# Kernel optimization log

Measured on AMD Instinct MI355X. Metric: run time of the kernel, lower is better.

The kernel has to match this reference:

```python
import jax, jax.numpy as jnp
import numpy as np

N, B, SDIM, ADIM, HID, HEADS = 8, 32768, 128, 16, 128, 4
AD = HID // HEADS  # attend_dim = 32
IDIM = SDIM + ADIM


def setup_inputs() -> dict:
    key = jax.random.key(0)
    ks = jax.random.split(key, 16)
    nrm = jax.random.normal
    return {
        "states": nrm(ks[0], (N, B, SDIM), jnp.float32),
        "actions": nrm(ks[1], (N, B, ADIM), jnp.float32),
        # per-agent critic encoder (Linear(idim, hid) + ReLU)
        "We": nrm(ks[2], (N, IDIM, HID), jnp.float32) * 0.05,
        "be": nrm(ks[3], (N, HID), jnp.float32) * 0.05,
        # per-agent state encoder (Linear(sdim, hid) + ReLU)
        "Ws": nrm(ks[4], (N, SDIM, HID), jnp.float32) * 0.05,
        "bs": nrm(ks[5], (N, HID), jnp.float32) * 0.05,
        # per-head extractors (shared across agents)
        "Wk": nrm(ks[6], (HEADS, HID, AD), jnp.float32) * 0.05,  # bias=False
        "Wq": nrm(ks[7], (HEADS, HID, AD), jnp.float32) * 0.05,  # bias=False
        "Wv": nrm(ks[8], (HEADS, HID, AD), jnp.float32) * 0.05,
        "bv": nrm(ks[9], (HEADS, AD), jnp.float32) * 0.05,
        # per-agent critic head: Linear(2*hid, hid) + ReLU + Linear(hid, adim)
        "Wc1": nrm(ks[10], (N, 2 * HID, HID), jnp.float32) * 0.05,
        "bc1": nrm(ks[11], (N, HID), jnp.float32) * 0.05,
        "Wc2": nrm(ks[12], (N, HID, ADIM), jnp.float32) * 0.05,
        "bc2": nrm(ks[13], (N, ADIM), jnp.float32) * 0.05,
    }


def reference(states, actions, We, be, Ws, bs, Wk, Wq, Wv, bv, Wc1, bc1, Wc2, bc2):
    # encoders
    inp = jnp.concatenate([states, actions], axis=-1)                      # [N,B,idim]
    sa_enc = jax.nn.relu(jnp.einsum('nbi,nih->nbh', inp, We) + be[:, None, :])
    s_enc = jax.nn.relu(jnp.einsum('nbs,nsh->nbh', states, Ws) + bs[:, None, :])
    # per-head keys/values/selectors; k = head index
    K = jnp.einsum('nbh,khd->knbd', sa_enc, Wk)                            # [H,N,B,ad]
    V = jax.nn.relu(jnp.einsum('nbh,khd->knbd', sa_enc, Wv) + bv[:, None, None, :])
    Q = jnp.einsum('nbh,khd->knbd', s_enc, Wq)
    # attention logits: selector of agent i dotted with key of agent j
    logits = jnp.einsum('kibd,kjbd->kbij', Q, K) / np.sqrt(AD).astype(np.float32)
    # exclude-self masking (equivalent to stacking keys with j != i)
    self_mask = jnp.eye(N, dtype=bool)                                     # [N,N]
    masked = jnp.where(self_mask[None, None, :, :], jnp.float32(-1e9), logits)
    attn = jax.nn.softmax(masked, axis=-1)                                 # [H,B,N,N]
    other = jnp.einsum('kbij,kjbd->ikbd', attn, V)                         # [N,H,B,ad]
    other = other.transpose(0, 2, 1, 3).reshape(N, B, HEADS * AD)          # head-order concat
    # per-agent critic MLP
    critic_in = jnp.concatenate([s_enc, other], axis=-1)                   # [N,B,2*hid]
    h1 = jax.nn.relu(jnp.einsum('nbc,nch->nbh', critic_in, Wc1) + bc1[:, None, :])
    all_q = jnp.einsum('nbh,nha->nba', h1, Wc2) + bc2[:, None, :]          # [N,B,adim]
    int_acs = jnp.argmax(actions, axis=-1)                                 # [N,B]
    q = jnp.take_along_axis(all_q, int_acs[..., None], axis=-1)            # [N,B,1]
    return q
```

## Files before the change

kernel.cpp:

```cpp
#include <hip/hip_runtime.h>

#define NAG 8
#define BB 32768
#define SDIM 128
#define ADIM 16
#define HID 128
#define IDIM 144

typedef unsigned short u16;
typedef unsigned int u32;
typedef __attribute__((ext_vector_type(8))) short short8;
typedef __attribute__((ext_vector_type(4))) float floatx4;

__device__ __forceinline__ u16 f2bf(float f) {
  u32 u = __float_as_uint(f);
  u32 r = (u + 0x7FFFu + ((u >> 16) & 1u)) >> 16;
  return (u16)r;
}
__device__ __forceinline__ float bflo(u32 u) { return __uint_as_float(u << 16); }
__device__ __forceinline__ float bfhi(u32 u) { return __uint_as_float(u & 0xFFFF0000u); }


__global__ void prep_kernel(const float* __restrict__ We, const float* __restrict__ Ws,
                            const float* __restrict__ Wk, const float* __restrict__ Wq,
                            const float* __restrict__ Wv, const float* __restrict__ Wc1,
                            u16* __restrict__ ws) {
  int idx = blockIdx.x * 256 + threadIdx.x;
  const float* src;
  u16* dst;
  int e, Kreal, mode = 0;
  if (idx < 163840) {
    int a = idx / 20480; e = idx % 20480;
    src = We + a * (IDIM * HID); dst = ws + a * 20480; Kreal = IDIM;
  } else if (idx < 294912) {
    int r = idx - 163840; int a = r >> 14; e = r & 16383;
    src = Ws + a * 16384; dst = ws + 163840 + a * 16384; Kreal = 128;
  } else if (idx < 311296) {
    e = idx - 294912; src = Wk; dst = ws + 294912; Kreal = 128; mode = 1;
  } else if (idx < 327680) {
    e = idx - 311296; src = Wv; dst = ws + 311296; Kreal = 128; mode = 1;
  } else if (idx < 344064) {
    e = idx - 327680; src = Wq; dst = ws + 327680; Kreal = 128; mode = 1;
  } else if (idx < 606208) {
    int r = idx - 344064; int a = r >> 15; e = r & 32767;
    src = Wc1 + a * 32768; dst = ws + 344064 + a * 32768; Kreal = 256;
  } else {
    return;
  }
  int j = e & 7, lane = (e >> 3) & 63, ct = (e >> 9) & 7, kc = e >> 12;
  int k = kc * 32 + ((lane >> 4) << 3) + j;
  int c = ct * 16 + (lane & 15);
  float val = 0.f;
  if (k < Kreal)
    val = mode ? src[((c >> 5) * 128 + k) * 32 + (c & 31)]
               : src[k * 128 + c];
  dst[e] = f2bf(val);
}

template <int NKC>
__device__ __forceinline__ void gemm8(const u16* A, const int astride, const u16* W,
                                      const int wave, const int lane, floatx4* acc) {
  const int arow = wave * 16 + (lane & 15);
  const int koff = (lane >> 4) << 3;
#pragma unroll
  for (int kc = 0; kc < NKC; ++kc) {
    short8 a = *(const short8*)&A[arow * astride + kc * 32 + koff];
#pragma unroll
    for (int ct = 0; ct < 8; ++ct) {
      short8 b = *(const short8*)&W[kc * 4096 + ct * 512 + lane * 8];
      acc[ct] = __builtin_amdgcn_mfma_f32_16x16x32_bf16(a, b, acc[ct], 0, 0, 0);
    }
  }
}

__global__ __launch_bounds__(512) void k1_kernel(
    const float* __restrict__ states, const float* __restrict__ actions,
    const float* __restrict__ be, const float* __restrict__ bs, const float* __restrict__ bv,
    const u16* __restrict__ wsbase,
    u16* __restrict__ Kbuf, u16* __restrict__ Vbuf, u16* __restrict__ Qbuf,
    u16* __restrict__ CI) {
  __shared__ __align__(16) u16 Alds[128 * 168];
  __shared__ __align__(16) u16 Wb[20480];
  __shared__ __align__(16) u16 E1[128 * 136];
  __shared__ __align__(16) u16 E2[128 * 136];

  const int tid = threadIdx.x, lane = tid & 63, wave = tid >> 6;
  const int n = blockIdx.y;
  const size_t b0 = (size_t)blockIdx.x * 128;
  const int colb = lane & 15;
  const int rowl = wave * 16 + ((lane >> 4) << 2);

  const u16* WeP = wsbase;
  const u16* WsP = wsbase + 163840;
  const u16* WkP = wsbase + 294912;
  const u16* WvP = wsbase + 311296;
  const u16* WqP = wsbase + 327680;

  {
    const float4* sp = (const float4*)(states + ((size_t)n * BB + b0) * SDIM);
#pragma unroll
    for (int it = 0; it < 8; ++it) {
      int c = tid + it * 512;
      float4 v = sp[c];
      int row = c >> 5, col = (c & 31) << 2;
      *(uint2*)&Alds[row * 168 + col] =
          make_uint2((u32)f2bf(v.x) | ((u32)f2bf(v.y) << 16),
                     (u32)f2bf(v.z) | ((u32)f2bf(v.w) << 16));
    }
    const float4* apt = (const float4*)(actions + ((size_t)n * BB + b0) * ADIM);
    {
      float4 v = apt[tid];
      int row = tid >> 2, col = 128 + ((tid & 3) << 2);
      *(uint2*)&Alds[row * 168 + col] =
          make_uint2((u32)f2bf(v.x) | ((u32)f2bf(v.y) << 16),
                     (u32)f2bf(v.z) | ((u32)f2bf(v.w) << 16));
    }
    {
      int row = tid >> 2, col = 144 + ((tid & 3) << 2);
      *(uint2*)&Alds[row * 168 + col] = make_uint2(0u, 0u);
    }
    const uint4* s4 = (const uint4*)(WeP + (size_t)n * 20480);
    uint4* d4 = (uint4*)Wb;
#pragma unroll
    for (int it = 0; it < 5; ++it) d4[tid + it * 512] = s4[tid + it * 512];
  }
  __syncthreads();

  floatx4 acc[8];

#pragma unroll
  for (int ct = 0; ct < 8; ++ct) acc[ct] = (floatx4){0.f, 0.f, 0.f, 0.f};
  gemm8<5>(Alds, 168, Wb, wave, lane, acc);
#pragma unroll
  for (int ct = 0; ct < 8; ++ct) {
    int col = ct * 16 + colb;
    float bb = be[n * HID + col];
#pragma unroll
    for (int r = 0; r < 4; ++r)
      E1[(rowl + r) * 136 + col] = f2bf(fmaxf(acc[ct][r] + bb, 0.f));
  }
  __syncthreads();
  {
    const uint4* s4 = (const uint4*)(WsP + (size_t)n * 16384);
    uint4* d4 = (uint4*)Wb;
#pragma unroll
    for (int it = 0; it < 4; ++it) d4[tid + it * 512] = s4[tid + it * 512];
  }
  __syncthreads();

#pragma unroll
  for (int ct = 0; ct < 8; ++ct) acc[ct] = (floatx4){0.f, 0.f, 0.f, 0.f};
  gemm8<4>(Alds, 168, Wb, wave, lane, acc);
#pragma unroll
  for (int ct = 0; ct < 8; ++ct) {
    int col = ct * 16 + colb;
    float bb = bs[n * HID + col];
#pragma unroll
    for (int r = 0; r < 4; ++r) {
      u16 u = f2bf(fmaxf(acc[ct][r] + bb, 0.f));
      E2[(rowl + r) * 136 + col] = u;
      CI[((size_t)n * BB + b0 + rowl + r) * 256 + col] = u;
    }
  }
  __syncthreads();
  {
    const uint4* s4 = (const uint4*)WkP;
    uint4* d4 = (uint4*)Wb;
#pragma unroll
    for (int it = 0; it < 4; ++it) d4[tid + it * 512] = s4[tid + it * 512];
  }
  __syncthreads();

#pragma unroll
  for (int ct = 0; ct < 8; ++ct) acc[ct] = (floatx4){0.f, 0.f, 0.f, 0.f};
  gemm8<4>(E1, 136, Wb, wave, lane, acc);
#pragma unroll
  for (int ct = 0; ct < 8; ++ct) {
    int col = ct * 16 + colb;
#pragma unroll
    for (int r = 0; r < 4; ++r)
      Kbuf[((size_t)n * BB + b0 + rowl + r) * HID + col] = f2bf(acc[ct][r]);
  }
  __syncthreads();
  {
    const uint4* s4 = (const uint4*)WvP;
    uint4* d4 = (uint4*)Wb;
#pragma unroll
    for (int it = 0; it < 4; ++it) d4[tid + it * 512] = s4[tid + it * 512];
  }
  __syncthreads();

#pragma unroll
  for (int ct = 0; ct < 8; ++ct) acc[ct] = (floatx4){0.f, 0.f, 0.f, 0.f};
  gemm8<4>(E1, 136, Wb, wave, lane, acc);
#pragma unroll
  for (int ct = 0; ct < 8; ++ct) {
    int col = ct * 16 + colb;
    float bb = bv[col];
#pragma unroll
    for (int r = 0; r < 4; ++r)
      Vbuf[((size_t)n * BB + b0 + rowl + r) * HID + col] = f2bf(fmaxf(acc[ct][r] + bb, 0.f));
  }
  __syncthreads();
  {
    const uint4* s4 = (const uint4*)WqP;
    uint4* d4 = (uint4*)Wb;
#pragma unroll
    for (int it = 0; it < 4; ++it) d4[tid + it * 512] = s4[tid + it * 512];
  }
  __syncthreads();

#pragma unroll
  for (int ct = 0; ct < 8; ++ct) acc[ct] = (floatx4){0.f, 0.f, 0.f, 0.f};
  gemm8<4>(E2, 136, Wb, wave, lane, acc);
#pragma unroll
  for (int ct = 0; ct < 8; ++ct) {
    int col = ct * 16 + colb;
#pragma unroll
    for (int r = 0; r < 4; ++r)
      Qbuf[((size_t)n * BB + b0 + rowl + r) * HID + col] = f2bf(acc[ct][r]);
  }
}

__global__ __launch_bounds__(512, 4) void k2_kernel(const u16* __restrict__ Kb,
                                                    const u16* __restrict__ Vb,
                                                    const u16* __restrict__ Qb,
                                                    u16* __restrict__ CI) {
  __shared__ __align__(16) u16 Ksh[8 * 16 * 128];
  __shared__ __align__(16) u16 Vsh[8 * 16 * 128];

  const int tid = threadIdx.x;
  const int i = tid >> 6;
  const int lane = tid & 63;
  const int h = lane >> 4;
  const int b = lane & 15;
  const size_t b0 = (size_t)blockIdx.x * 16;
  const float scale = 0.17677669529663687f;

  {
    uint4* kd = (uint4*)Ksh;
    uint4* vd = (uint4*)Vsh;
#pragma unroll
    for (int it = 0; it < 4; ++it) {
      int l = tid + it * 512;
      int j = l >> 8, bs_ = (l >> 4) & 15, t = l & 15;
      size_t gidx = ((size_t)j * BB + b0 + bs_) * 16 + t;
      int slot = (t + bs_) & 15;
      int didx = (j * 16 + bs_) * 16 + slot;
      kd[didx] = ((const uint4*)Kb)[gidx];
      vd[didx] = ((const uint4*)Vb)[gidx];
    }
  }
  __syncthreads();

  float q[32];
  {
    const u32* qp = (const u32*)(Qb + ((size_t)i * BB + b0 + b) * HID + h * 32);
#pragma unroll
    for (int t = 0; t < 16; ++t) {
      u32 u = qp[t];
      q[2 * t] = bflo(u);
      q[2 * t + 1] = bfhi(u);
    }
  }

  float lg[8];
#pragma unroll
  for (int j = 0; j < 8; ++j) {
    if (j != i) {
      float acc = 0.f;
#pragma unroll
      for (int c = 0; c < 4; ++c) {
        int slot = ((h * 4 + c) + b) & 15;
        uint4 kv = *(const uint4*)&Ksh[((j * 16 + b) * 16 + slot) * 8];
        const u32 kw[4] = {kv.x, kv.y, kv.z, kv.w};
#pragma unroll
        for (int t = 0; t < 4; ++t) {
          int d = c * 8 + t * 2;
          acc = fmaf(bflo(kw[t]), q[d], acc);
          acc = fmaf(bfhi(kw[t]), q[d + 1], acc);
        }
      }
      lg[j] = acc * scale;
    } else {
      lg[j] = -1e9f;
    }
  }

  float m = lg[0];
#pragma unroll
  for (int j = 1; j < 8; ++j) m = fmaxf(m, lg[j]);
  float p[8], s = 0.f;
#pragma unroll
  for (int j = 0; j < 8; ++j) {
    p[j] = __expf(lg[j] - m);
    s += p[j];
  }
  const float inv = 1.f / s;

  float o[32];
#pragma unroll
  for (int d = 0; d < 32; ++d) o[d] = 0.f;
#pragma unroll
  for (int j = 0; j < 8; ++j) {
    if (j == i) continue;
    const float pj = p[j] * inv;
#pragma unroll
    for (int c = 0; c < 4; ++c) {
      int slot = ((h * 4 + c) + b) & 15;
      uint4 vv = *(const uint4*)&Vsh[((j * 16 + b) * 16 + slot) * 8];
      const u32 vw[4] = {vv.x, vv.y, vv.z, vv.w};
#pragma unroll
      for (int t = 0; t < 4; ++t) {
        int d = c * 8 + t * 2;
        o[d] = fmaf(pj, bflo(vw[t]), o[d]);
        o[d + 1] = fmaf(pj, bfhi(vw[t]), o[d + 1]);
      }
    }
  }

  u32 ow[16];
#pragma unroll
  for (int t = 0; t < 16; ++t)
    ow[t] = (u32)f2bf(o[2 * t]) | ((u32)f2bf(o[2 * t + 1]) << 16);
  uint4* op = (uint4*)(CI + ((size_t)i * BB + b0 + b) * 256 + 128 + h * 32);
  op[0] = make_uint4(ow[0], ow[1], ow[2], ow[3]);
  op[1] = make_uint4(ow[4], ow[5], ow[6], ow[7]);
  op[2] = make_uint4(ow[8], ow[9], ow[10], ow[11]);
  op[3] = make_uint4(ow[12], ow[13], ow[14], ow[15]);
}

__global__ __launch_bounds__(512) void k3_kernel(
    const u16* __restrict__ CI, const u16* __restrict__ Wc1P, const float* __restrict__ bc1,
    const float* __restrict__ Wc2, const float* __restrict__ bc2,
    const float* __restrict__ actions, float* __restrict__ out) {
  __shared__ __align__(16) u16 Alds[128 * 264];
  __shared__ __align__(16) u16 Wb[32768];
  __shared__ __align__(16) float Wc2s[2048];

  const int tid = threadIdx.x, lane = tid & 63, wave = tid >> 6;
  const int n = blockIdx.y;
  const size_t b0 = (size_t)blockIdx.x * 128;
  const int colb = lane & 15;
  const int rowl = wave * 16 + ((lane >> 4) << 2);

  {
    const uint4* src = (const uint4*)(CI + ((size_t)n * BB + b0) * 256);
    uint4* dstA = (uint4*)Alds;
#pragma unroll
    for (int it = 0; it < 8; ++it) {
      int c = tid + it * 512;
      int row = c >> 5, c16 = c & 31;
      dstA[row * 33 + c16] = src[c];
    }
    const uint4* wsrc = (const uint4*)(Wc1P + (size_t)n * 32768);
    uint4* wdst = (uint4*)Wb;
#pragma unroll
    for (int it = 0; it < 8; ++it) wdst[tid + it * 512] = wsrc[tid + it * 512];
    ((float4*)Wc2s)[tid] = ((const float4*)(Wc2 + n * 2048))[tid];
  }
  __syncthreads();

  floatx4 acc[8];
#pragma unroll
  for (int ct = 0; ct < 8; ++ct) acc[ct] = (floatx4){0.f, 0.f, 0.f, 0.f};
  gemm8<8>(Alds, 264, Wb, wave, lane, acc);
  __syncthreads();

#pragma unroll
  for (int ct = 0; ct < 8; ++ct) {
    int col = ct * 16 + colb;
    float bb = bc1[n * HID + col];
#pragma unroll
    for (int r = 0; r < 4; ++r) {
      float v = fmaxf(acc[ct][r] + bb, 0.f);
      Alds[(rowl + r) * 136 + col] = f2bf(v);
    }
  }
  __syncthreads();

  {
    const int bloc = tid >> 2, part = tid & 3;
    const size_t b = b0 + bloc;
    const float* ap = actions + ((size_t)n * BB + b) * ADIM;
    int am = 0;
    float mv = ap[0];
#pragma unroll
    for (int t = 1; t < 16; ++t) {
      float v = ap[t];
      if (v > mv) { mv = v; am = t; }
    }
    float a2 = 0.f;
    const int cb = part * 32;
#pragma unroll
    for (int c2 = 0; c2 < 32; ++c2) {
      float hv = __uint_as_float((u32)Alds[bloc * 136 + cb + c2] << 16);
      a2 = fmaf(hv, Wc2s[(cb + c2) * 16 + am], a2);
    }
    a2 += __shfl_xor(a2, 1);
    a2 += __shfl_xor(a2, 2);
    if (part == 0) out[(size_t)n * BB + b] = a2 + bc2[n * ADIM + am];
  }
}

extern "C" void kernel_launch(void* const* d_in, const int* in_sizes, int n_in,
                              void* d_out, int out_size, void* d_ws, size_t ws_size,
                              hipStream_t stream) {
  const float* states  = (const float*)d_in[0];
  const float* actions = (const float*)d_in[1];
  const float* We  = (const float*)d_in[2];
  const float* be  = (const float*)d_in[3];
  const float* Ws  = (const float*)d_in[4];
  const float* bs  = (const float*)d_in[5];
  const float* Wk  = (const float*)d_in[6];
  const float* Wq  = (const float*)d_in[7];
  const float* Wv  = (const float*)d_in[8];
  const float* bv  = (const float*)d_in[9];
  const float* Wc1 = (const float*)d_in[10];
  const float* bc1 = (const float*)d_in[11];
  const float* Wc2 = (const float*)d_in[12];
  const float* bc2 = (const float*)d_in[13];
  float* out = (float*)d_out;
  u16* ws = (u16*)d_ws;

  u16* Kbuf = ws + 606208;
  u16* Vbuf = ws + 34160640;
  u16* Qbuf = ws + 67715072;
  u16* CI   = ws + 101269504;

  prep_kernel<<<2368, 256, 0, stream>>>(We, Ws, Wk, Wq, Wv, Wc1, ws);
  k1_kernel<<<dim3(256, 8), 512, 0, stream>>>(states, actions, be, bs, bv, ws,
                                              Kbuf, Vbuf, Qbuf, CI);
  k2_kernel<<<2048, 512, 0, stream>>>(Kbuf, Vbuf, Qbuf, CI);
  k3_kernel<<<dim3(256, 8), 512, 0, stream>>>(CI, ws + 344064, bc1, Wc2, bc2, actions, out);
}
```

Measured before the change: 448.9 us.

## Read MFMA weight fragments directly from global memory and shrink LDS footprint

The k1 and k3 kernels no longer stage weight matrices into shared memory. The pre-swizzled bf16 weight fragments are now read straight from global memory (through cache) inside the MFMA loop. This removes the per-GEMM copy-and-barrier steps and the large Wb LDS buffers. k1's GEMMs are reordered so one E buffer is reused, and launch bounds now request 4 blocks per CU to raise occupancy. The trade-off is more global/L2 traffic for weights on every k-chunk, plus possible register pressure under the tighter launch bound.

```diff
diff --git a/kernel.cpp b/kernel.cpp
--- a/kernel.cpp
+++ b/kernel.cpp
@@ -58,7 +58,8 @@
 }
 
 template <int NKC>
-__device__ __forceinline__ void gemm8(const u16* A, const int astride, const u16* W,
+__device__ __forceinline__ void gemm8(const u16* A, const int astride,
+                                      const u16* __restrict__ W,
                                       const int wave, const int lane, floatx4* acc) {
   const int arow = wave * 16 + (lane & 15);
   const int koff = (lane >> 4) << 3;
@@ -73,16 +74,14 @@
   }
 }
 
-__global__ __launch_bounds__(512) void k1_kernel(
+__global__ __launch_bounds__(512, 4) void k1_kernel(
     const float* __restrict__ states, const float* __restrict__ actions,
     const float* __restrict__ be, const float* __restrict__ bs, const float* __restrict__ bv,
     const u16* __restrict__ wsbase,
     u16* __restrict__ Kbuf, u16* __restrict__ Vbuf, u16* __restrict__ Qbuf,
     u16* __restrict__ CI) {
-  __shared__ __align__(16) u16 Alds[128 * 168];
-  __shared__ __align__(16) u16 Wb[20480];
-  __shared__ __align__(16) u16 E1[128 * 136];
-  __shared__ __align__(16) u16 E2[128 * 136];
+  __shared__ __align__(16) u16 Alds[128 * 160];
+  __shared__ __align__(16) u16 Ebuf[128 * 136];
 
   const int tid = threadIdx.x, lane = tid & 63, wave = tid >> 6;
   const int n = blockIdx.y;
@@ -90,8 +89,8 @@
   const int colb = lane & 15;
   const int rowl = wave * 16 + ((lane >> 4) << 2);
 
-  const u16* WeP = wsbase;
-  const u16* WsP = wsbase + 163840;
+  const u16* WeP = wsbase + (size_t)n * 20480;
+  const u16* WsP = wsbase + 163840 + (size_t)n * 16384;
   const u16* WkP = wsbase + 294912;
   const u16* WvP = wsbase + 311296;
   const u16* WqP = wsbase + 327680;
@@ -103,7 +102,7 @@
       int c = tid + it * 512;
       float4 v = sp[c];
       int row = c >> 5, col = (c & 31) << 2;
-      *(uint2*)&Alds[row * 168 + col] =
+      *(uint2*)&Alds[row * 160 + col] =
           make_uint2((u32)f2bf(v.x) | ((u32)f2bf(v.y) << 16),
                      (u32)f2bf(v.z) | ((u32)f2bf(v.w) << 16));
     }
@@ -111,18 +110,14 @@
     {
       float4 v = apt[tid];
       int row = tid >> 2, col = 128 + ((tid & 3) << 2);
-      *(uint2*)&Alds[row * 168 + col] =
+      *(uint2*)&Alds[row * 160 + col] =
           make_uint2((u32)f2bf(v.x) | ((u32)f2bf(v.y) << 16),
                      (u32)f2bf(v.z) | ((u32)f2bf(v.w) << 16));
     }
     {
       int row = tid >> 2, col = 144 + ((tid & 3) << 2);
-      *(uint2*)&Alds[row * 168 + col] = make_uint2(0u, 0u);
-    }
-    const uint4* s4 = (const uint4*)(WeP + (size_t)n * 20480);
-    uint4* d4 = (uint4*)Wb;
-#pragma unroll
-    for (int it = 0; it < 5; ++it) d4[tid + it * 512] = s4[tid + it * 512];
+      *(uint2*)&Alds[row * 160 + col] = make_uint2(0u, 0u);
+    }
   }
   __syncthreads();
 
@@ -130,27 +125,44 @@
 
 #pragma unroll
   for (int ct = 0; ct < 8; ++ct) acc[ct] = (floatx4){0.f, 0.f, 0.f, 0.f};
-  gemm8<5>(Alds, 168, Wb, wave, lane, acc);
+  gemm8<5>(Alds, 160, WeP, wave, lane, acc);
 #pragma unroll
   for (int ct = 0; ct < 8; ++ct) {
     int col = ct * 16 + colb;
     float bb = be[n * HID + col];
 #pragma unroll
     for (int r = 0; r < 4; ++r)
-      E1[(rowl + r) * 136 + col] = f2bf(fmaxf(acc[ct][r] + bb, 0.f));
-  }
-  __syncthreads();
-  {
-    const uint4* s4 = (const uint4*)(WsP + (size_t)n * 16384);
-    uint4* d4 = (uint4*)Wb;
-#pragma unroll
-    for (int it = 0; it < 4; ++it) d4[tid + it * 512] = s4[tid + it * 512];
-  }
-  __syncthreads();
-
-#pragma unroll
-  for (int ct = 0; ct < 8; ++ct) acc[ct] = (floatx4){0.f, 0.f, 0.f, 0.f};
-  gemm8<4>(Alds, 168, Wb, wave, lane, acc);
+      Ebuf[(rowl + r) * 136 + col] = f2bf(fmaxf(acc[ct][r] + bb, 0.f));
+  }
+  __syncthreads();
+
+#pragma unroll
+  for (int ct = 0; ct < 8; ++ct) acc[ct] = (floatx4){0.f, 0.f, 0.f, 0.f};
+  gemm8<4>(Ebuf, 136, WkP, wave, lane, acc);
+#pragma unroll
+  for (int ct = 0; ct < 8; ++ct) {
+    int col = ct * 16 + colb;
+#pragma unroll
+    for (int r = 0; r < 4; ++r)
+      Kbuf[((size_t)n * BB + b0 + rowl + r) * HID + col] = f2bf(acc[ct][r]);
+  }
+
+#pragma unroll
+  for (int ct = 0; ct < 8; ++ct) acc[ct] = (floatx4){0.f, 0.f, 0.f, 0.f};
+  gemm8<4>(Ebuf, 136, WvP, wave, lane, acc);
+#pragma unroll
+  for (int ct = 0; ct < 8; ++ct) {
+    int col = ct * 16 + colb;
+    float bb = bv[col];
+#pragma unroll
+    for (int r = 0; r < 4; ++r)
+      Vbuf[((size_t)n * BB + b0 + rowl + r) * HID + col] = f2bf(fmaxf(acc[ct][r] + bb, 0.f));
+  }
+
+#pragma unroll
+  for (int ct = 0; ct < 8; ++ct) acc[ct] = (floatx4){0.f, 0.f, 0.f, 0.f};
+  gemm8<4>(Alds, 160, WsP, wave, lane, acc);
+  u16 e2u[32];
 #pragma unroll
   for (int ct = 0; ct < 8; ++ct) {
     int col = ct * 16 + colb;
@@ -158,61 +170,24 @@
 #pragma unroll
     for (int r = 0; r < 4; ++r) {
       u16 u = f2bf(fmaxf(acc[ct][r] + bb, 0.f));
-      E2[(rowl + r) * 136 + col] = u;
+      e2u[ct * 4 + r] = u;
       CI[((size_t)n * BB + b0 + rowl + r) * 256 + col] = u;
     }
   }
   __syncthreads();
-  {
-    const uint4* s4 = (const uint4*)WkP;
-    uint4* d4 = (uint4*)Wb;
-#pragma unroll
-    for (int it = 0; it < 4; ++it) d4[tid + it * 512] = s4[tid + it * 512];
-  }
-  __syncthreads();
-
-#pragma unroll
-  for (int ct = 0; ct < 8; ++ct) acc[ct] = (floatx4){0.f, 0.f, 0.f, 0.f};
-  gemm8<4>(E1, 136, Wb, wave, lane, acc);
+
 #pragma unroll
   for (int ct = 0; ct < 8; ++ct) {
     int col = ct * 16 + colb;
 #pragma unroll
     for (int r = 0; r < 4; ++r)
-      Kbuf[((size_t)n * BB + b0 + rowl + r) * HID + col] = f2bf(acc[ct][r]);
-  }
-  __syncthreads();
-  {
-    const uint4* s4 = (const uint4*)WvP;
-    uint4* d4 = (uint4*)Wb;
-#pragma unroll
-    for (int it = 0; it < 4; ++it) d4[tid + it * 512] = s4[tid + it * 512];
-  }
-  __syncthreads();
-
-#pragma unroll
-  for (int ct = 0; ct < 8; ++ct) acc[ct] = (floatx4){0.f, 0.f, 0.f, 0.f};
-  gemm8<4>(E1, 136, Wb, wave, lane, acc);
-#pragma unroll
-  for (int ct = 0; ct < 8; ++ct) {
-    int col = ct * 16 + colb;
-    float bb = bv[col];
-#pragma unroll
-    for (int r = 0; r < 4; ++r)
-      Vbuf[((size_t)n * BB + b0 + rowl + r) * HID + col] = f2bf(fmaxf(acc[ct][r] + bb, 0.f));
-  }
-  __syncthreads();
-  {
-    const uint4* s4 = (const uint4*)WqP;
-    uint4* d4 = (uint4*)Wb;
-#pragma unroll
-    for (int it = 0; it < 4; ++it) d4[tid + it * 512] = s4[tid + it * 512];
-  }
-  __syncthreads();
-
-#pragma unroll
-  for (int ct = 0; ct < 8; ++ct) acc[ct] = (floatx4){0.f, 0.f, 0.f, 0.f};
-  gemm8<4>(E2, 136, Wb, wave, lane, acc);
+      Ebuf[(rowl + r) * 136 + col] = e2u[ct * 4 + r];
+  }
+  __syncthreads();
+
+#pragma unroll
+  for (int ct = 0; ct < 8; ++ct) acc[ct] = (floatx4){0.f, 0.f, 0.f, 0.f};
+  gemm8<4>(Ebuf, 136, WqP, wave, lane, acc);
 #pragma unroll
   for (int ct = 0; ct < 8; ++ct) {
     int col = ct * 16 + colb;
@@ -330,12 +305,11 @@
   op[3] = make_uint4(ow[12], ow[13], ow[14], ow[15]);
 }
 
-__global__ __launch_bounds__(512) void k3_kernel(
+__global__ __launch_bounds__(512, 4) void k3_kernel(
     const u16* __restrict__ CI, const u16* __restrict__ Wc1P, const float* __restrict__ bc1,
     const float* __restrict__ Wc2, const float* __restrict__ bc2,
     const float* __restrict__ actions, float* __restrict__ out) {
   __shared__ __align__(16) u16 Alds[128 * 264];
-  __shared__ __align__(16) u16 Wb[32768];
   __shared__ __align__(16) float Wc2s[2048];
 
   const int tid = threadIdx.x, lane = tid & 63, wave = tid >> 6;
@@ -353,10 +327,6 @@
       int row = c >> 5, c16 = c & 31;
       dstA[row * 33 + c16] = src[c];
     }
-    const uint4* wsrc = (const uint4*)(Wc1P + (size_t)n * 32768);
-    uint4* wdst = (uint4*)Wb;
-#pragma unroll
-    for (int it = 0; it < 8; ++it) wdst[tid + it * 512] = wsrc[tid + it * 512];
     ((float4*)Wc2s)[tid] = ((const float4*)(Wc2 + n * 2048))[tid];
   }
   __syncthreads();
@@ -364,7 +334,7 @@
   floatx4 acc[8];
 #pragma unroll
   for (int ct = 0; ct < 8; ++ct) acc[ct] = (floatx4){0.f, 0.f, 0.f, 0.f};
-  gemm8<8>(Alds, 264, Wb, wave, lane, acc);
+  gemm8<8>(Alds, 264, Wc1P + (size_t)n * 32768, wave, lane, acc);
   __syncthreads();
 
 #pragma unroll
```

After: 493.3 us. 9.9% more time.
